# Kernel tuning notes

Hardware: AMD Instinct MI355X
Metric: run time of the kernel (lower is better)

The kernel has to match this reference:

```python
import jax, jax.numpy as jnp
import numpy as np

N_NODES = 50000
D_MODEL = 128
N_EDGES = 600000
HIDDEN = 128
EDGE_FEAT = 2 * D_MODEL + 2  # 258


def setup_inputs() -> dict:
    key = jax.random.key(0)
    k = jax.random.split(key, 8)
    H = jax.random.normal(k[0], (N_NODES, D_MODEL), dtype=jnp.float32)
    edge_index = jax.random.randint(k[1], (2, N_EDGES), 0, N_NODES, dtype=jnp.int64)
    S_e = jax.random.uniform(k[2], (N_EDGES,), dtype=jnp.float32)
    F_e = jax.random.uniform(k[3], (N_EDGES,), dtype=jnp.float32)
    W1 = jax.random.normal(k[4], (EDGE_FEAT, HIDDEN), dtype=jnp.float32) * (1.0 / np.sqrt(EDGE_FEAT))
    b1 = jnp.zeros((HIDDEN,), dtype=jnp.float32)
    W2 = jax.random.normal(k[5], (HIDDEN, 1), dtype=jnp.float32) * (1.0 / np.sqrt(HIDDEN))
    b2 = jnp.zeros((1,), dtype=jnp.float32)
    return {"H": H, "edge_index": edge_index, "S_e": S_e, "F_e": F_e,
            "W1": W1, "b1": b1, "W2": W2, "b2": b2}


def reference(H, edge_index, S_e, F_e, W1, b1, W2, b2):
    # Gather endpoint node features: [E, D]
    H_u = H[edge_index[0]]
    H_v = H[edge_index[1]]
    H_diff = jnp.abs(H_u - H_v)
    H_prod = H_u * H_v
    # [E, 2D+2]
    edge_features = jnp.concatenate(
        [H_diff, H_prod, S_e[:, None], F_e[:, None]], axis=1)
    # 2-layer MLP with SiLU (dropout is identity in eval mode)
    h = jax.nn.silu(edge_features @ W1 + b1)
    a_e = (h @ W2 + b2)[:, 0]  # [E]
    return a_e
```

## Files before the change

### kernel.cpp

```cpp
#include <hip/hip_runtime.h>


typedef _Float16       half8   __attribute__((ext_vector_type(8)));
typedef _Float16       half4v  __attribute__((ext_vector_type(4)));
typedef unsigned short ushort8 __attribute__((ext_vector_type(8)));
typedef float          f32x4   __attribute__((ext_vector_type(4)));

#define NSEG    8

__device__ __forceinline__ float silu_f(float x) {
    return x / (1.0f + __expf(-x));
}

__device__ __forceinline__ void canon(int u, int v, int& a, int& b) {
    const int sw = (u ^ v) & 1;
    a = sw ? v : u;
    b = sw ? u : v;
}


__global__ __launch_bounds__(256)
void cvt_zero_kernel(const float* __restrict__ H, _Float16* __restrict__ Hh,
                     int n4, int* __restrict__ zp, int nz) {
    int i = blockIdx.x * blockDim.x + threadIdx.x;
    if (i < nz) zp[i] = 0;
    if (i < n4) {
        const float4 f = ((const float4*)H)[i];
        half4v h;
        h[0] = (_Float16)f.x; h[1] = (_Float16)f.y;
        h[2] = (_Float16)f.z; h[3] = (_Float16)f.w;
        ((half4v*)Hh)[i] = h;
    }
}

__global__ __launch_bounds__(256)
void hist_kernel(const int* __restrict__ eidx, int* __restrict__ hist,
                 int E, int ASZ, int BBINS) {
    int e = blockIdx.x * blockDim.x + threadIdx.x;
    if (e < E) {
        int a, b;
        canon(eidx[e], eidx[E + e], a, b);
        atomicAdd(&hist[(a / ASZ) * BBINS + (b >> 3)], 1);
    }
}

__global__ __launch_bounds__(256)
void scan1_kernel(int* __restrict__ hist, int* __restrict__ bsum, int NB) {
    __shared__ int s[256];
    const int t = threadIdx.x;
    const int i = blockIdx.x * 256 + t;
    const int v = (i < NB) ? hist[i] : 0;
    s[t] = v;
    __syncthreads();
    for (int off = 1; off < 256; off <<= 1) {
        const int x = (t >= off) ? s[t - off] : 0;
        __syncthreads();
        s[t] += x;
        __syncthreads();
    }
    if (i < NB) hist[i] = s[t] - v;
    if (t == 255) bsum[blockIdx.x] = s[255];
}

__global__ __launch_bounds__(256)
void scan2_kernel(int* __restrict__ bsum, int nb1,
                  const int* __restrict__ hist, int* __restrict__ vbs,
                  int BBINS, int E) {
    __shared__ int s[256];
    const int t = threadIdx.x;
    const int v = (t < nb1) ? bsum[t] : 0;
    s[t] = v;
    __syncthreads();
    for (int off = 1; off < 256; off <<= 1) {
        const int x = (t >= off) ? s[t - off] : 0;
        __syncthreads();
        s[t] += x;
        __syncthreads();
    }
    if (t < nb1) bsum[t] = s[t] - v;
    __syncthreads();
    if (t < NSEG) {
        const int idx = t * BBINS;
        vbs[t] = hist[idx] + bsum[idx >> 8];
    } else if (t == NSEG) {
        vbs[NSEG] = E;
    }
}

__global__ __launch_bounds__(256)
void scatter_kernel(const int* __restrict__ eidx, const float* __restrict__ Se,
                    const float* __restrict__ Fe, int* __restrict__ ofs,
                    const int* __restrict__ bsum,
                    int4* __restrict__ recs, int E, int ASZ, int BBINS) {
    int e = blockIdx.x * blockDim.x + threadIdx.x;
    if (e < E) {
        int a, b;
        canon(eidx[e], eidx[E + e], a, b);
        const int key = (a / ASZ) * BBINS + (b >> 3);
        const int pos = atomicAdd(&ofs[key], 1) + bsum[key >> 8];
        _Float16 sh = (_Float16)Se[e];
        _Float16 fh = (_Float16)Fe[e];
        unsigned pk = (unsigned)*(unsigned short*)&sh
                    | ((unsigned)*(unsigned short*)&fh << 16);
        recs[pos] = make_int4(a, b, e, (int)pk);
    }
}


__device__ __forceinline__ void stage_w1(const float* __restrict__ W1,
                                         _Float16* __restrict__ w1t, int tid) {
    const int n = tid & 127;
    const int g = tid >> 7;
    #pragma unroll
    for (int i = 0; i < 8; ++i) {
        const int kb = g + (i << 2);
        half8 tmp;
        #pragma unroll
        for (int j = 0; j < 8; ++j) {
            const int kp  = (kb << 3) + j;
            const int c   = kp >> 5;
            const int k32 = kp & 31;
            const int src = ((c & 1) << 7) + ((c >> 1) << 5) + k32;
            tmp[j] = (_Float16)W1[src * 128 + n];
        }
        *(half8*)&w1t[n * 256 + ((kb ^ (n & 7)) << 3)] = tmp;
    }
}


__device__ __forceinline__ void edge_tile16(
    const _Float16* __restrict__ Hh, const int4* __restrict__ recs,
    const _Float16* __restrict__ w1t,
    const float* __restrict__ W1, const float* __restrict__ b1,
    const float* __restrict__ W2, float b2v, float* __restrict__ out,
    int ebase, int elim, int q, int cb, int swz)
{
    const int e = min(ebase + cb, elim - 1);
    const int4 r = recs[e];
    const int a = r.x, b = r.y, oe = r.z;
    const unsigned pk = (unsigned)r.w;
    const unsigned short sl = (unsigned short)(pk & 0xFFFF);
    const unsigned short fl = (unsigned short)(pk >> 16);
    const float Sf = (float)*(const _Float16*)&sl;
    const float Ff = (float)*(const _Float16*)&fl;

    const _Float16* up = Hh + (size_t)a * 128;
    const _Float16* vp = Hh + (size_t)b * 128;

    f32x4 acc[8];
    #pragma unroll
    for (int t = 0; t < 8; ++t) acc[t] = (f32x4){0.f, 0.f, 0.f, 0.f};

    #pragma unroll
    for (int c8 = 0; c8 < 4; ++c8) {
        const half8 u8 = *(const half8*)(up + (c8 << 5) + (q << 3));
        const half8 v8 = *(const half8*)(vp + (c8 << 5) + (q << 3));
        half8 d8 = u8 - v8;
        ushort8 du = *(ushort8*)&d8;
        du = du & (unsigned short)0x7FFF;
        const half8 ae = *(half8*)&du;
        const half8 ao = u8 * v8;

        const int kb0 = ((c8 << 3) + q) ^ swz;
        const int kb1 = ((c8 << 3) + 4 + q) ^ swz;
        #pragma unroll
        for (int t = 0; t < 8; ++t) {
            const half8 b0 = *(const half8*)&w1t[((t << 4) + cb) * 256 + (kb0 << 3)];
            acc[t] = __builtin_amdgcn_mfma_f32_16x16x32_f16(ae, b0, acc[t], 0, 0, 0);
        }
        #pragma unroll
        for (int t = 0; t < 8; ++t) {
            const half8 b1f = *(const half8*)&w1t[((t << 4) + cb) * 256 + (kb1 << 3)];
            acc[t] = __builtin_amdgcn_mfma_f32_16x16x32_f16(ao, b1f, acc[t], 0, 0, 0);
        }
    }

    float s_r[4], f_r[4]; int oe_r[4];
    #pragma unroll
    for (int rr = 0; rr < 4; ++rr) {
        const int src = (q << 2) + rr;
        s_r[rr]  = __shfl(Sf, src);
        f_r[rr]  = __shfl(Ff, src);
        oe_r[rr] = __shfl(oe, src);
    }

    float rs[4] = {0.f, 0.f, 0.f, 0.f};
    #pragma unroll
    for (int t = 0; t < 8; ++t) {
        const int col    = (t << 4) + cb;
        const float w256 = W1[32768 + col];
        const float w257 = W1[32896 + col];
        const float b1c  = b1[col];
        const float w2c  = W2[col];
        const f32x4 av = acc[t];
        #pragma unroll
        for (int rr = 0; rr < 4; ++rr)
            rs[rr] += silu_f(av[rr] + s_r[rr] * w256 + f_r[rr] * w257 + b1c) * w2c;
    }

    #pragma unroll
    for (int off = 1; off < 16; off <<= 1) {
        #pragma unroll
        for (int rr = 0; rr < 4; ++rr) rs[rr] += __shfl_xor(rs[rr], off);
    }

    if (cb == 0) {
        #pragma unroll
        for (int rr = 0; rr < 4; ++rr) {
            const int pe = ebase + (q << 2) + rr;
            if (pe < elim) out[oe_r[rr]] = rs[rr] + b2v;
        }
    }
}


__global__ __launch_bounds__(512, 4)
void edgegate_seg(const _Float16* __restrict__ Hh,
                  const int4*  __restrict__ recs,
                  const int*   __restrict__ vbs,
                  int*         __restrict__ ctr,
                  const float* __restrict__ W1,
                  const float* __restrict__ b1,
                  const float* __restrict__ W2,
                  const float* __restrict__ b2,
                  float*       __restrict__ out)
{
    __shared__ _Float16 w1t[128 * 256];
    __shared__ int tkt[2];
    const int tid = threadIdx.x;
    stage_w1(W1, w1t, tid);

    int xcd;
    asm volatile("s_getreg_b32 %0, hwreg(HW_REG_XCC_ID)" : "=s"(xcd));
    xcd &= (NSEG - 1);

    __syncthreads();

    const int lane = tid & 63;
    const int wave = tid >> 6;
    const int q    = lane >> 4;
    const int cb   = lane & 15;
    const int swz  = cb & 7;
    const float b2v = b2[0];

    int p = 0;
    for (int sidx = 0; sidx < NSEG; ++sidx) {
        const int seg = (xcd + sidx) & (NSEG - 1);
        const int vs  = vbs[seg];
        const int ve  = vbs[seg + 1];
        const int ner = ve - vs;
        if (ner <= 0) continue;
        const int Tt = (ner + 127) >> 7;

        while (true) {
            if (tid == 0) tkt[p] = atomicAdd(&ctr[seg], 1);
            __syncthreads();
            const int t0 = tkt[p];
            p ^= 1;
            if (t0 >= Tt) break;
            const int ebase = vs + (t0 << 7) + (wave << 4);
            edge_tile16(Hh, recs, w1t, W1, b1, W2, b2v, out, ebase, ve, q, cb, swz);
        }
    }
}


__global__ __launch_bounds__(512, 4)
void edgegate_fb(const float* __restrict__ H,
                 const _Float16* __restrict__ Hh,
                 const int*   __restrict__ eidx,
                 const float* __restrict__ Se,
                 const float* __restrict__ Fe,
                 const float* __restrict__ W1,
                 const float* __restrict__ b1,
                 const float* __restrict__ W2,
                 const float* __restrict__ b2,
                 float*       __restrict__ out,
                 int E, int ntiles, int useF16)
{
    __shared__ _Float16 w1t[128 * 256];
    const int tid = threadIdx.x;
    stage_w1(W1, w1t, tid);
    __syncthreads();

    const int lane = tid & 63;
    const int wave = tid >> 6;
    const int q    = lane >> 4;
    const int cb   = lane & 15;
    const int swz  = cb & 7;

    for (int tile = blockIdx.x; tile < ntiles; tile += gridDim.x) {
        const int ebase = tile * 128 + wave * 16;
        int e = ebase + cb;
        if (e >= E) e = E - 1;
        const int u = eidx[e];
        const int v = eidx[E + e];

        f32x4 acc[8];
        #pragma unroll
        for (int t = 0; t < 8; ++t) acc[t] = (f32x4){0.f, 0.f, 0.f, 0.f};

        #pragma unroll
        for (int c8 = 0; c8 < 4; ++c8) {
            half8 ae, ao;
            if (useF16) {
                const _Float16* up = Hh + (size_t)u * 128;
                const _Float16* vp = Hh + (size_t)v * 128;
                const half8 u8 = *(const half8*)(up + (c8 << 5) + (q << 3));
                const half8 v8 = *(const half8*)(vp + (c8 << 5) + (q << 3));
                half8 d8 = u8 - v8;
                ushort8 du = *(ushort8*)&d8;
                du = du & (unsigned short)0x7FFF;
                ae = *(half8*)&du;
                ao = u8 * v8;
            } else {
                const float* up = H + (size_t)u * 128;
                const float* vp = H + (size_t)v * 128;
                #pragma unroll
                for (int j = 0; j < 8; ++j) {
                    const float uu = up[(c8 << 5) + (q << 3) + j];
                    const float vv = vp[(c8 << 5) + (q << 3) + j];
                    ae[j] = (_Float16)fabsf(uu - vv);
                    ao[j] = (_Float16)(uu * vv);
                }
            }
            const int kb0 = ((c8 << 3) + q) ^ swz;
            const int kb1 = ((c8 << 3) + 4 + q) ^ swz;
            #pragma unroll
            for (int t = 0; t < 8; ++t) {
                const half8 b0 = *(const half8*)&w1t[((t << 4) + cb) * 256 + (kb0 << 3)];
                acc[t] = __builtin_amdgcn_mfma_f32_16x16x32_f16(ae, b0, acc[t], 0, 0, 0);
            }
            #pragma unroll
            for (int t = 0; t < 8; ++t) {
                const half8 b1f = *(const half8*)&w1t[((t << 4) + cb) * 256 + (kb1 << 3)];
                acc[t] = __builtin_amdgcn_mfma_f32_16x16x32_f16(ao, b1f, acc[t], 0, 0, 0);
            }
        }

        const int e0  = ebase + (q << 2);
        const int e0c = (e0 + 3 < E) ? e0 : (E - 4);
        const float4 s4 = *(const float4*)(Se + e0c);
        const float4 f4 = *(const float4*)(Fe + e0c);

        float rs0 = 0.f, rs1 = 0.f, rs2 = 0.f, rs3 = 0.f;
        #pragma unroll
        for (int t = 0; t < 8; ++t) {
            const int col    = (t << 4) + cb;
            const float w256 = W1[32768 + col];
            const float w257 = W1[32896 + col];
            const float b1c  = b1[col];
            const float w2c  = W2[col];
            const f32x4 av = acc[t];
            rs0 += silu_f(av[0] + s4.x * w256 + f4.x * w257 + b1c) * w2c;
            rs1 += silu_f(av[1] + s4.y * w256 + f4.y * w257 + b1c) * w2c;
            rs2 += silu_f(av[2] + s4.z * w256 + f4.z * w257 + b1c) * w2c;
            rs3 += silu_f(av[3] + s4.w * w256 + f4.w * w257 + b1c) * w2c;
        }
        #pragma unroll
        for (int off = 1; off < 16; off <<= 1) {
            rs0 += __shfl_xor(rs0, off);
            rs1 += __shfl_xor(rs1, off);
            rs2 += __shfl_xor(rs2, off);
            rs3 += __shfl_xor(rs3, off);
        }
        if (cb == 0 && e0 < E) {
            const float b2v = b2[0];
            out[e0]     = rs0 + b2v;
            out[e0 + 1] = rs1 + b2v;
            out[e0 + 2] = rs2 + b2v;
            out[e0 + 3] = rs3 + b2v;
        }
    }
}


static inline size_t align256(size_t x) { return (x + 255) & ~(size_t)255; }

extern "C" void kernel_launch(void* const* d_in, const int* in_sizes, int n_in,
                              void* d_out, int out_size, void* d_ws, size_t ws_size,
                              hipStream_t stream)
{
    const float* H    = (const float*)d_in[0];
    const int*   eidx = (const int*)  d_in[1];
    const float* Se   = (const float*)d_in[2];
    const float* Fe   = (const float*)d_in[3];
    const float* W1   = (const float*)d_in[4];
    const float* b1   = (const float*)d_in[5];
    const float* W2   = (const float*)d_in[6];
    const float* b2   = (const float*)d_in[7];
    float* out = (float*)d_out;

    const int nH     = in_sizes[0];
    const int nNodes = nH / 128;
    const int E      = in_sizes[2];
    const int n4     = nH / 4;
    const int ntiles = (E + 127) / 128;

    const int ASZ   = (nNodes + NSEG - 1) / NSEG;
    const int BBINS = (nNodes + 7) >> 3;
    const int NB    = NSEG * BBINS;
    const int nb1   = (NB + 255) / 256;

    const size_t hhB    = (size_t)nH * sizeof(_Float16);
    const size_t off_g  = align256(hhB);
    const size_t off_bs = align256(off_g + (size_t)(NB + 8) * 4);
    const size_t off_vb = align256(off_bs + 256 * 4);
    const size_t off_r  = align256(off_vb + 16 * 4);
    const size_t need   = off_r + (size_t)E * sizeof(int4);

    if (ws_size >= need && nb1 <= 256) {
        _Float16* Hh   = (_Float16*)((char*)d_ws);
        int*      hist = (int*)     ((char*)d_ws + off_g);
        int*      ctr  = hist + NB;
        int*      bsum = (int*)     ((char*)d_ws + off_bs);
        int*      vbs  = (int*)     ((char*)d_ws + off_vb);
        int4*     recs = (int4*)    ((char*)d_ws + off_r);

        hipLaunchKernelGGL(cvt_zero_kernel, dim3((n4 + 255) / 256), dim3(256),
                           0, stream, H, Hh, n4, hist, NB + 8);
        hipLaunchKernelGGL(hist_kernel, dim3((E + 255) / 256), dim3(256),
                           0, stream, eidx, hist, E, ASZ, BBINS);
        hipLaunchKernelGGL(scan1_kernel, dim3(nb1), dim3(256), 0, stream,
                           hist, bsum, NB);
        hipLaunchKernelGGL(scan2_kernel, dim3(1), dim3(256), 0, stream,
                           bsum, nb1, hist, vbs, BBINS, E);
        hipLaunchKernelGGL(scatter_kernel, dim3((E + 255) / 256), dim3(256),
                           0, stream, eidx, Se, Fe, hist, bsum, recs,
                           E, ASZ, BBINS);
        hipLaunchKernelGGL(edgegate_seg, dim3(512), dim3(512), 0, stream,
                           Hh, recs, vbs, ctr, W1, b1, W2, b2, out);
    } else if (ws_size >= hhB) {
        _Float16* Hh = (_Float16*)d_ws;
        const int grid = (512 < ntiles) ? 512 : ntiles;
        hipLaunchKernelGGL(cvt_zero_kernel, dim3((n4 + 255) / 256), dim3(256),
                           0, stream, H, Hh, n4, (int*)nullptr, 0);
        hipLaunchKernelGGL(edgegate_fb, dim3(grid), dim3(512), 0, stream,
                           H, Hh, eidx, Se, Fe, W1, b1, W2, b2, out, E, ntiles, 1);
    } else {
        const int grid = (512 < ntiles) ? 512 : ntiles;
        hipLaunchKernelGGL(edgegate_fb, dim3(grid), dim3(512), 0, stream,
                           H, (const _Float16*)nullptr, eidx, Se, Fe, W1, b1, W2, b2,
                           out, E, ntiles, 0);
    }
}
```

Baseline: 291.2 us.

## Fold edge scalars into MFMA, per-wave work stealing, fuse cvt with histogram

The S_e, F_e and bias terms now go through an extra K=32 MFMA step against a padded LDS W1 slab (stride 288), replacing per-column scalar global loads in the epilogue. W2 is preloaded into registers. Each wave now grabs 32-edge tiles from the atomic counter on its own, instead of the block-wide ticket with __syncthreads. The FP16 conversion is merged into the histogram kernel, with a memset zeroing the histogram. The cost is one more MFMA group per tile, more per-wave atomics, and a larger LDS footprint that may reduce occupancy.

```diff
diff --git a/kernel.cpp b/kernel.cpp
--- a/kernel.cpp
+++ b/kernel.cpp
@@ -6,7 +6,8 @@
 typedef unsigned short ushort8 __attribute__((ext_vector_type(8)));
 typedef float          f32x4   __attribute__((ext_vector_type(4)));
 
-#define NSEG    8
+#define NSEG       8
+#define W1T_STRIDE 288
 
 __device__ __forceinline__ float silu_f(float x) {
     return x / (1.0f + __expf(-x));
@@ -20,10 +21,10 @@
 
 
 __global__ __launch_bounds__(256)
-void cvt_zero_kernel(const float* __restrict__ H, _Float16* __restrict__ Hh,
-                     int n4, int* __restrict__ zp, int nz) {
+void cvt_hist_kernel(const float* __restrict__ H, _Float16* __restrict__ Hh,
+                     int n4, const int* __restrict__ eidx,
+                     int* __restrict__ hist, int E, int ASZ, int BBINS) {
     int i = blockIdx.x * blockDim.x + threadIdx.x;
-    if (i < nz) zp[i] = 0;
     if (i < n4) {
         const float4 f = ((const float4*)H)[i];
         half4v h;
@@ -31,15 +32,9 @@
         h[2] = (_Float16)f.z; h[3] = (_Float16)f.w;
         ((half4v*)Hh)[i] = h;
     }
-}
-
-__global__ __launch_bounds__(256)
-void hist_kernel(const int* __restrict__ eidx, int* __restrict__ hist,
-                 int E, int ASZ, int BBINS) {
-    int e = blockIdx.x * blockDim.x + threadIdx.x;
-    if (e < E) {
+    if (i < E) {
         int a, b;
-        canon(eidx[e], eidx[E + e], a, b);
+        canon(eidx[i], eidx[E + i], a, b);
         atomicAdd(&hist[(a / ASZ) * BBINS + (b >> 3)], 1);
     }
 }
@@ -108,22 +103,37 @@
 
 
 __device__ __forceinline__ void stage_w1(const float* __restrict__ W1,
+                                         const float* __restrict__ b1,
                                          _Float16* __restrict__ w1t, int tid) {
     const int n = tid & 127;
     const int g = tid >> 7;
     #pragma unroll
-    for (int i = 0; i < 8; ++i) {
+    for (int i = 0; i < 9; ++i) {
         const int kb = g + (i << 2);
         half8 tmp;
-        #pragma unroll
-        for (int j = 0; j < 8; ++j) {
-            const int kp  = (kb << 3) + j;
-            const int c   = kp >> 5;
-            const int k32 = kp & 31;
-            const int src = ((c & 1) << 7) + ((c >> 1) << 5) + k32;
-            tmp[j] = (_Float16)W1[src * 128 + n];
-        }
-        *(half8*)&w1t[n * 256 + ((kb ^ (n & 7)) << 3)] = tmp;
+        if (kb < 32) {
+            #pragma unroll
+            for (int j = 0; j < 8; ++j) {
+                const int kp  = (kb << 3) + j;
+                const int c   = kp >> 5;
+                const int k32 = kp & 31;
+                const int src = ((c & 1) << 7) + ((c >> 1) << 5) + k32;
+                tmp[j] = (_Float16)W1[src * 128 + n];
+            }
+            *(half8*)&w1t[n * W1T_STRIDE + ((kb ^ (n & 7)) << 3)] = tmp;
+        } else {
+            const int k32b = (kb - 32) << 3;
+            #pragma unroll
+            for (int j = 0; j < 8; ++j) {
+                const int k32 = k32b + j;
+                float v = 0.f;
+                if (k32 == 0)      v = W1[32768 + n];
+                else if (k32 == 1) v = W1[32896 + n];
+                else if (k32 == 2) v = b1[n];
+                tmp[j] = (_Float16)v;
+            }
+            *(half8*)&w1t[n * W1T_STRIDE + (kb << 3)] = tmp;
+        }
     }
 }
 
@@ -131,18 +141,16 @@
 __device__ __forceinline__ void edge_tile16(
     const _Float16* __restrict__ Hh, const int4* __restrict__ recs,
     const _Float16* __restrict__ w1t,
-    const float* __restrict__ W1, const float* __restrict__ b1,
-    const float* __restrict__ W2, float b2v, float* __restrict__ out,
+    f32x4 w2a, f32x4 w2b, float b2v, float* __restrict__ out,
     int ebase, int elim, int q, int cb, int swz)
 {
+    if (ebase >= elim) return;
     const int e = min(ebase + cb, elim - 1);
     const int4 r = recs[e];
     const int a = r.x, b = r.y, oe = r.z;
     const unsigned pk = (unsigned)r.w;
     const unsigned short sl = (unsigned short)(pk & 0xFFFF);
     const unsigned short fl = (unsigned short)(pk >> 16);
-    const float Sf = (float)*(const _Float16*)&sl;
-    const float Ff = (float)*(const _Float16*)&fl;
 
     const _Float16* up = Hh + (size_t)a * 128;
     const _Float16* vp = Hh + (size_t)b * 128;
@@ -165,37 +173,42 @@
         const int kb1 = ((c8 << 3) + 4 + q) ^ swz;
         #pragma unroll
         for (int t = 0; t < 8; ++t) {
-            const half8 b0 = *(const half8*)&w1t[((t << 4) + cb) * 256 + (kb0 << 3)];
+            const half8 b0 = *(const half8*)&w1t[((t << 4) + cb) * W1T_STRIDE + (kb0 << 3)];
             acc[t] = __builtin_amdgcn_mfma_f32_16x16x32_f16(ae, b0, acc[t], 0, 0, 0);
         }
         #pragma unroll
         for (int t = 0; t < 8; ++t) {
-            const half8 b1f = *(const half8*)&w1t[((t << 4) + cb) * 256 + (kb1 << 3)];
+            const half8 b1f = *(const half8*)&w1t[((t << 4) + cb) * W1T_STRIDE + (kb1 << 3)];
             acc[t] = __builtin_amdgcn_mfma_f32_16x16x32_f16(ao, b1f, acc[t], 0, 0, 0);
         }
     }
 
-    float s_r[4], f_r[4]; int oe_r[4];
-    #pragma unroll
-    for (int rr = 0; rr < 4; ++rr) {
-        const int src = (q << 2) + rr;
-        s_r[rr]  = __shfl(Sf, src);
-        f_r[rr]  = __shfl(Ff, src);
-        oe_r[rr] = __shfl(oe, src);
-    }
+    half8 aE;
+    #pragma unroll
+    for (int j = 0; j < 8; ++j) aE[j] = (_Float16)0.f;
+    if (q == 0) {
+        aE[0] = *(const _Float16*)&sl;
+        aE[1] = *(const _Float16*)&fl;
+        aE[2] = (_Float16)1.0f;
+    }
+    #pragma unroll
+    for (int t = 0; t < 8; ++t) {
+        const half8 bE = *(const half8*)&w1t[((t << 4) + cb) * W1T_STRIDE + ((32 + q) << 3)];
+        acc[t] = __builtin_amdgcn_mfma_f32_16x16x32_f16(aE, bE, acc[t], 0, 0, 0);
+    }
+
+    int oe_r[4];
+    #pragma unroll
+    for (int rr = 0; rr < 4; ++rr) oe_r[rr] = __shfl(oe, (q << 2) + rr);
 
     float rs[4] = {0.f, 0.f, 0.f, 0.f};
     #pragma unroll
     for (int t = 0; t < 8; ++t) {
-        const int col    = (t << 4) + cb;
-        const float w256 = W1[32768 + col];
-        const float w257 = W1[32896 + col];
-        const float b1c  = b1[col];
-        const float w2c  = W2[col];
+        const float w2c = (t < 4) ? w2a[t] : w2b[t - 4];
         const f32x4 av = acc[t];
         #pragma unroll
         for (int rr = 0; rr < 4; ++rr)
-            rs[rr] += silu_f(av[rr] + s_r[rr] * w256 + f_r[rr] * w257 + b1c) * w2c;
+            rs[rr] += silu_f(av[rr]) * w2c;
     }
 
     #pragma unroll
@@ -225,41 +238,46 @@
                   const float* __restrict__ b2,
                   float*       __restrict__ out)
 {
-    __shared__ _Float16 w1t[128 * 256];
-    __shared__ int tkt[2];
+    __shared__ _Float16 w1t[128 * W1T_STRIDE];
     const int tid = threadIdx.x;
-    stage_w1(W1, w1t, tid);
+    stage_w1(W1, b1, w1t, tid);
 
     int xcd;
     asm volatile("s_getreg_b32 %0, hwreg(HW_REG_XCC_ID)" : "=s"(xcd));
     xcd &= (NSEG - 1);
 
-    __syncthreads();
-
     const int lane = tid & 63;
-    const int wave = tid >> 6;
     const int q    = lane >> 4;
     const int cb   = lane & 15;
     const int swz  = cb & 7;
     const float b2v = b2[0];
-
-    int p = 0;
+    f32x4 w2a, w2b;
+    #pragma unroll
+    for (int t = 0; t < 4; ++t) {
+        w2a[t] = W2[(t << 4) + cb];
+        w2b[t] = W2[((t + 4) << 4) + cb];
+    }
+
+    __syncthreads();
+
     for (int sidx = 0; sidx < NSEG; ++sidx) {
         const int seg = (xcd + sidx) & (NSEG - 1);
         const int vs  = vbs[seg];
         const int ve  = vbs[seg + 1];
         const int ner = ve - vs;
         if (ner <= 0) continue;
-        const int Tt = (ner + 127) >> 7;
-
-        while (true) {
-            if (tid == 0) tkt[p] = atomicAdd(&ctr[seg], 1);
-            __syncthreads();
-            const int t0 = tkt[p];
-            p ^= 1;
-            if (t0 >= Tt) break;
-            const int ebase = vs + (t0 << 7) + (wave << 4);
-            edge_tile16(Hh, recs, w1t, W1, b1, W2, b2v, out, ebase, ve, q, cb, swz);
+        const int Tt = (ner + 31) >> 5;
+
+        int tn = 0;
+        if (lane == 0) tn = atomicAdd(&ctr[seg], 1);
+        tn = __shfl(tn, 0);
+        while (tn < Tt) {
+            int tnext = 0;
+            if (lane == 0) tnext = atomicAdd(&ctr[seg], 1);
+            const int ebase = vs + (tn << 5);
+            edge_tile16(Hh, recs, w1t, w2a, w2b, b2v, out, ebase,      ve, q, cb, swz);
+            edge_tile16(Hh, recs, w1t, w2a, w2b, b2v, out, ebase + 16, ve, q, cb, swz);
+            tn = __shfl(tnext, 0);
         }
     }
 }
@@ -278,16 +296,24 @@
                  float*       __restrict__ out,
                  int E, int ntiles, int useF16)
 {
-    __shared__ _Float16 w1t[128 * 256];
+    __shared__ _Float16 w1t[128 * W1T_STRIDE];
     const int tid = threadIdx.x;
-    stage_w1(W1, w1t, tid);
-    __syncthreads();
+    stage_w1(W1, b1, w1t, tid);
 
     const int lane = tid & 63;
     const int wave = tid >> 6;
     const int q    = lane >> 4;
     const int cb   = lane & 15;
     const int swz  = cb & 7;
+    const float b2v = b2[0];
+    f32x4 w2a, w2b;
+    #pragma unroll
+    for (int t = 0; t < 4; ++t) {
+        w2a[t] = W2[(t << 4) + cb];
+        w2b[t] = W2[((t + 4) << 4) + cb];
+    }
+
+    __syncthreads();
 
     for (int tile = blockIdx.x; tile < ntiles; tile += gridDim.x) {
         const int ebase = tile * 128 + wave * 16;
@@ -295,6 +321,8 @@
         if (e >= E) e = E - 1;
         const int u = eidx[e];
         const int v = eidx[E + e];
+        const float sfe = Se[e];
+        const float ffe = Fe[e];
 
         f32x4 acc[8];
         #pragma unroll
@@ -328,48 +356,52 @@
             const int kb1 = ((c8 << 3) + 4 + q) ^ swz;
             #pragma unroll
             for (int t = 0; t < 8; ++t) {
-                const half8 b0 = *(const half8*)&w1t[((t << 4) + cb) * 256 + (kb0 << 3)];
+                const half8 b0 = *(const half8*)&w1t[((t << 4) + cb) * W1T_STRIDE + (kb0 << 3)];
                 acc[t] = __builtin_amdgcn_mfma_f32_16x16x32_f16(ae, b0, acc[t], 0, 0, 0);
             }
             #pragma unroll
             for (int t = 0; t < 8; ++t) {
-                const half8 b1f = *(const half8*)&w1t[((t << 4) + cb) * 256 + (kb1 << 3)];
+                const half8 b1f = *(const half8*)&w1t[((t << 4) + cb) * W1T_STRIDE + (kb1 << 3)];
                 acc[t] = __builtin_amdgcn_mfma_f32_16x16x32_f16(ao, b1f, acc[t], 0, 0, 0);
             }
         }
 
-        const int e0  = ebase + (q << 2);
-        const int e0c = (e0 + 3 < E) ? e0 : (E - 4);
-        const float4 s4 = *(const float4*)(Se + e0c);
-        const float4 f4 = *(const float4*)(Fe + e0c);
-
-        float rs0 = 0.f, rs1 = 0.f, rs2 = 0.f, rs3 = 0.f;
+        half8 aE;
+        #pragma unroll
+        for (int j = 0; j < 8; ++j) aE[j] = (_Float16)0.f;
+        if (q == 0) {
+            aE[0] = (_Float16)sfe;
+            aE[1] = (_Float16)ffe;
+            aE[2] = (_Float16)1.0f;
+        }
         #pragma unroll
         for (int t = 0; t < 8; ++t) {
-            const int col    = (t << 4) + cb;
-            const float w256 = W1[32768 + col];
-            const float w257 = W1[32896 + col];
-            const float b1c  = b1[col];
-            const float w2c  = W2[col];
+            const half8 bE = *(const half8*)&w1t[((t << 4) + cb) * W1T_STRIDE + ((32 + q) << 3)];
+            acc[t] = __builtin_amdgcn_mfma_f32_16x16x32_f16(aE, bE, acc[t], 0, 0, 0);
+        }
+
+        float rs[4] = {0.f, 0.f, 0.f, 0.f};
+        #pragma unroll
+        for (int t = 0; t < 8; ++t) {
+            const float w2c = (t < 4) ? w2a[t] : w2b[t - 4];
             const f32x4 av = acc[t];
-            rs0 += silu_f(av[0] + s4.x * w256 + f4.x * w257 + b1c) * w2c;
-            rs1 += silu_f(av[1] + s4.y * w256 + f4.y * w257 + b1c) * w2c;
-            rs2 += silu_f(av[2] + s4.z * w256 + f4.z * w257 + b1c) * w2c;
-            rs3 += silu_f(av[3] + s4.w * w256 + f4.w * w257 + b1c) * w2c;
+            #pragma unroll
+            for (int rr = 0; rr < 4; ++rr)
+                rs[rr] += silu_f(av[rr]) * w2c;
         }
         #pragma unroll
         for (int off = 1; off < 16; off <<= 1) {
-            rs0 += __shfl_xor(rs0, off);
-            rs1 += __shfl_xor(rs1, off);
-            rs2 += __shfl_xor(rs2, off);
-            rs3 += __shfl_xor(rs3, off);
-        }
-        if (cb == 0 && e0 < E) {
-            const float b2v = b2[0];
-            out[e0]     = rs0 + b2v;
-            out[e0 + 1] = rs1 + b2v;
-            out[e0 + 2] = rs2 + b2v;
-            out[e0 + 3] = rs3 + b2v;
+            #pragma unroll
+            for (int rr = 0; rr < 4; ++rr) rs[rr] += __shfl_xor(rs[rr], off);
+        }
+
+        const int e0 = ebase + (q << 2);
+        if (cb == 0) {
+            #pragma unroll
+            for (int rr = 0; rr < 4; ++rr) {
+                const int pe = e0 + rr;
+                if (pe < E) out[pe] = rs[rr] + b2v;
+            }
         }
     }
 }
@@ -417,10 +449,10 @@
         int*      vbs  = (int*)     ((char*)d_ws + off_vb);
         int4*     recs = (int4*)    ((char*)d_ws + off_r);
 
-        hipLaunchKernelGGL(cvt_zero_kernel, dim3((n4 + 255) / 256), dim3(256),
-                           0, stream, H, Hh, n4, hist, NB + 8);
-        hipLaunchKernelGGL(hist_kernel, dim3((E + 255) / 256), dim3(256),
-                           0, stream, eidx, hist, E, ASZ, BBINS);
+        const int ncvh = (n4 > E) ? n4 : E;
+        hipMemsetAsync(hist, 0, (size_t)(NB + 8) * sizeof(int), stream);
+        hipLaunchKernelGGL(cvt_hist_kernel, dim3((ncvh + 255) / 256), dim3(256),
+                           0, stream, H, Hh, n4, eidx, hist, E, ASZ, BBINS);
         hipLaunchKernelGGL(scan1_kernel, dim3(nb1), dim3(256), 0, stream,
                            hist, bsum, NB);
         hipLaunchKernelGGL(scan2_kernel, dim3(1), dim3(256), 0, stream,
@@ -433,8 +465,8 @@
     } else if (ws_size >= hhB) {
         _Float16* Hh = (_Float16*)d_ws;
         const int grid = (512 < ntiles) ? 512 : ntiles;
-        hipLaunchKernelGGL(cvt_zero_kernel, dim3((n4 + 255) / 256), dim3(256),
-                           0, stream, H, Hh, n4, (int*)nullptr, 0);
+        hipLaunchKernelGGL(cvt_hist_kernel, dim3((n4 + 255) / 256), dim3(256),
+                           0, stream, H, Hh, n4, eidx, (int*)nullptr, 0, 1, 1);
         hipLaunchKernelGGL(edgegate_fb, dim3(grid), dim3(512), 0, stream,
                            H, Hh, eidx, Se, Fe, W1, b1, W2, b2, out, E, ntiles, 1);
     } else {
```

After: 756.5 us. 2.6x slower.
